# Kernel tuning notes

Measured on AMD Instinct MI355X. Metric: run time of the kernel, lower is better.

The kernel has to match this reference:

```python
import jax, jax.numpy as jnp
import numpy as np

H, K, D = 24, 2, 128          # query heads, kv heads, head_size
HIDDEN = H * D                # 3072
ROPE_THETA = 10000.0


def setup_inputs() -> dict:
    key = jax.random.key(0)
    ks = jax.random.split(key, 6)
    B, S = 2, 2048
    T = B * S
    hidden_states = jax.random.normal(ks[0], (T, HIDDEN), dtype=jnp.float32)
    w_qkv = jax.random.normal(ks[1], ((H + 2 * K) * D, HIDDEN), dtype=jnp.float32) * (HIDDEN ** -0.5)
    b_qkv = jax.random.normal(ks[2], ((H + 2 * K) * D,), dtype=jnp.float32) * 0.02
    w_o = jax.random.normal(ks[3], (HIDDEN, H * D), dtype=jnp.float32) * (HIDDEN ** -0.5)
    b_o = jax.random.normal(ks[4], (HIDDEN,), dtype=jnp.float32) * 0.02
    # rotary tables: positions restart per sequence (flash-varlen prefill layout)
    pos = jnp.tile(jnp.arange(S, dtype=jnp.float32), B)            # [T]
    inv_freq = 1.0 / (ROPE_THETA ** (jnp.arange(0, D, 2, dtype=jnp.float32) / D))  # [D/2]
    freqs = pos[:, None] * inv_freq[None, :]                        # [T, D/2]
    return {
        "hidden_states": hidden_states,
        "w_qkv": w_qkv, "b_qkv": b_qkv,
        "w_o": w_o, "b_o": b_o,
        "cos": jnp.cos(freqs), "sin": jnp.sin(freqs),
        "seq_len": S, "window": 1024,
    }


def _rope(x, cos, sin):
    # rotate-half (neox) style, as in TGI PositionRotaryEmbedding
    half = x.shape[-1] // 2
    x1, x2 = x[..., :half], x[..., half:]
    c, s = cos[:, None, :], sin[:, None, :]   # broadcast over head dim
    return jnp.concatenate([x1 * c - x2 * s, x2 * c + x1 * s], axis=-1)


def reference(hidden_states, w_qkv, b_qkv, w_o, b_o, cos, sin, seq_len, window):
    T = hidden_states.shape[0]
    B = T // seq_len
    scale = D ** -0.5

    # fused QKV projection
    qkv = hidden_states @ w_qkv.T + b_qkv                 # [T, (H+2K)*D]
    q = qkv[:, : H * D].reshape(T, H, D)
    kv = qkv[:, H * D:].reshape(T, 2, K, D)
    k, v = kv[:, 0], kv[:, 1]                             # [T, K, D]

    q = _rope(q, cos, sin)
    k = _rope(k, cos, sin)

    # GQA: expand kv heads to query heads
    groups = H // K
    qb = q.reshape(B, seq_len, H, D)
    kb = jnp.repeat(k.reshape(B, seq_len, K, D), groups, axis=2)  # [B,S,H,D]
    vb = jnp.repeat(v.reshape(B, seq_len, K, D), groups, axis=2)

    scores = jnp.einsum("bqhd,bkhd->bhqk", qb, kb) * scale        # [B,H,S,S]
    idx = jnp.arange(seq_len)
    delta = idx[:, None] - idx[None, :]
    mask = (delta >= 0) & (delta < window)                        # causal + sliding window
    scores = jnp.where(mask[None, None], scores, jnp.float32(-1e9))
    attn = jax.nn.softmax(scores, axis=-1)
    out = jnp.einsum("bhqk,bkhd->bqhd", attn, vb).reshape(T, H * D)
    return out @ w_o.T + b_o
```

## Files before the change

### kernel.cpp

```cpp
#include <hip/hip_runtime.h>
#include <hip/hip_bf16.h>

typedef __attribute__((ext_vector_type(8))) short bf16x8;
typedef __attribute__((ext_vector_type(4))) float f32x4;

__device__ __forceinline__ short f2bf_bits(float f) {
    __hip_bfloat16 h = __float2bfloat16(f);
    short s;
    __builtin_memcpy(&s, &h, 2);
    return s;
}

__device__ __forceinline__ float bf_bits2f(short s) {
    unsigned int u = ((unsigned int)(unsigned short)s) << 16;
    float f;
    __builtin_memcpy(&f, &u, 4);
    return f;
}

__device__ __forceinline__ bf16x8 load8(const float* p) {
    float4 a = *(const float4*)p;
    float4 b = *(const float4*)(p + 4);
    bf16x8 r;
    r[0] = f2bf_bits(a.x); r[1] = f2bf_bits(a.y);
    r[2] = f2bf_bits(a.z); r[3] = f2bf_bits(a.w);
    r[4] = f2bf_bits(b.x); r[5] = f2bf_bits(b.y);
    r[6] = f2bf_bits(b.z); r[7] = f2bf_bits(b.w);
    return r;
}
__device__ __forceinline__ bf16x8 load8(const __hip_bfloat16* p) {
    return *(const bf16x8*)p;
}

__device__ __forceinline__ void store_out(__hip_bfloat16* p, float v) {
    *p = __float2bfloat16(v);
}
__device__ __forceinline__ void store_out(float* p, float v) { *p = v; }

__global__ void cvt3_f32_bf16(const float* __restrict__ a, short* __restrict__ da, int na8,
                              const float* __restrict__ b, short* __restrict__ db, int nb8,
                              const float* __restrict__ c, short* __restrict__ dc, int nc8) {
    int i = blockIdx.x * 256 + threadIdx.x;
    if (i < na8) {
        *(bf16x8*)(da + (size_t)i * 8) = load8(a + (size_t)i * 8);
    } else if ((i -= na8) < nb8) {
        *(bf16x8*)(db + (size_t)i * 8) = load8(b + (size_t)i * 8);
    } else if ((i -= nb8) < nc8) {
        *(bf16x8*)(dc + (size_t)i * 8) = load8(c + (size_t)i * 8);
    }
}

#define GB_REG 65536

__device__ __forceinline__ int half_off(int buf, int half) {
    return buf * 32768 + half * 16384;
}

template <typename TC>
__global__ __launch_bounds__(512) void gemm256(
    const __hip_bfloat16* __restrict__ A, const __hip_bfloat16* __restrict__ B,
    const float* __restrict__ bias, TC* __restrict__ C, int M, int N, int K)
{
    __shared__ char smem[131072];

    const int tid  = threadIdx.x;
    const int lane = tid & 63;
    const int wid  = tid >> 6;
    const int quad = lane >> 4;
    const int m16  = lane & 15;
    const int wmg  = wid >> 2;
    const int wng  = wid & 3;
    const int bhalf = wng >> 1;
    const int bsub  = (wng & 1) * 4;

    const int gx  = gridDim.x;
    const int nwg = gx * gridDim.y;
    int lin = blockIdx.y * gx + blockIdx.x;
    if ((nwg & 7) == 0) {
        int q = nwg >> 3;
        lin = (lin & 7) * q + (lin >> 3);
    }
    const int bn = lin % gx, bm = lin / gx;
    const int mBase = bm * 256, nBase = bn * 256;

    const int roff = (m16 << 6) | ((quad * 16) ^ (((m16 >> 1) & 3) << 4));

    int r_s[2], c_s[2];
    #pragma unroll
    for (int l = 0; l < 2; ++l) {
        int sub = l * 8 + wid;
        int r16 = (tid >> 2) & 15;
        int cb  = ((tid & 3) * 16) ^ (((r16 >> 1) & 3) << 4);
        r_s[l] = (sub >> 1) * 16 + r16;
        c_s[l] = (sub & 1) * 32 + (cb >> 1);
    }

    const __hip_bfloat16* Ab = A + (size_t)mBase * K;
    const __hip_bfloat16* Bb = B + (size_t)nBase * K;

    auto stage = [&](int region, const __hip_bfloat16* base, int buf, int half, int tile) {
        const __hip_bfloat16* gb = base + (size_t)(half * 128) * K + tile * 64;
        #pragma unroll
        for (int l = 0; l < 2; ++l) {
            const __hip_bfloat16* g = gb + (size_t)r_s[l] * K + c_s[l];
            short* lb = (short*)(smem + region + half_off(buf, half) + l * 8192 + wid * 1024);
            __builtin_amdgcn_global_load_lds(
                (__attribute__((address_space(1))) void*)g,
                (__attribute__((address_space(3))) void*)lb, 16, 0, 0);
        }
    };

    f32x4 acc[8][4] = {};
    bf16x8 afr[4][2];
    bf16x8 bfr[2][2][2];

    auto LD_A = [&](int buf, int g) {
        const char* base = smem + half_off(buf, wmg) + (g ? 8192 : 0);
        #pragma unroll
        for (int m = 0; m < 4; ++m)
            #pragma unroll
            for (int ks = 0; ks < 2; ++ks)
                afr[m][ks] = *(const bf16x8*)(base + ((m * 2 + ks) << 10) + roff);
    };
    auto LD_B = [&](int buf, int g) {
        const char* base = smem + GB_REG + half_off(buf, bhalf) + ((bsub + g * 2) << 11);
        #pragma unroll
        for (int j = 0; j < 2; ++j)
            #pragma unroll
            for (int ks = 0; ks < 2; ++ks)
                bfr[g][j][ks] = *(const bf16x8*)(base + ((j * 2 + ks) << 10) + roff);
    };
    auto MM = [&](int mo, int g) {
        #pragma unroll
        for (int m = 0; m < 4; ++m)
            #pragma unroll
            for (int j = 0; j < 2; ++j)
                #pragma unroll
                for (int ks = 0; ks < 2; ++ks)
                    acc[mo + m][g * 2 + j] = __builtin_amdgcn_mfma_f32_16x16x32_bf16(
                        afr[m][ks], bfr[g][j][ks], acc[mo + m][g * 2 + j], 0, 0, 0);
    };

#define SBAR() __builtin_amdgcn_s_barrier()
#define WAIT_LGKM0() do { asm volatile("s_waitcnt lgkmcnt(0)" ::: "memory"); \
                          __builtin_amdgcn_sched_barrier(0); } while (0)
#define WAIT_VM4()   do { asm volatile("s_waitcnt vmcnt(4)"   ::: "memory"); \
                          __builtin_amdgcn_sched_barrier(0); } while (0)

    const int NT = K >> 6;

    stage(GB_REG, Bb, 0, 0, 0);
    stage(0,      Ab, 0, 0, 0);
    stage(GB_REG, Bb, 0, 1, 0);
    stage(0,      Ab, 0, 1, 0);
    stage(GB_REG, Bb, 1, 0, 1);
    stage(0,      Ab, 1, 0, 1);
    WAIT_VM4();
    SBAR();

    for (int i = 0; i < (NT >> 1); ++i) {
        const int to = 2 * i + 1;
        const int t2 = min(2 * i + 2, NT - 1);
        const int t3 = min(2 * i + 3, NT - 1);
        LD_A(0, 0); LD_B(0, 0);
        stage(GB_REG, Bb, 1, 1, to);
        SBAR(); WAIT_LGKM0();
        __builtin_amdgcn_s_setprio(1); MM(0, 0); __builtin_amdgcn_s_setprio(0);
        SBAR();
        LD_B(0, 1);
        stage(0, Ab, 1, 1, to);
        SBAR(); WAIT_LGKM0();
        __builtin_amdgcn_s_setprio(1); MM(0, 1); __builtin_amdgcn_s_setprio(0);
        SBAR();
        LD_A(0, 1);
        stage(GB_REG, Bb, 0, 0, t2);
        SBAR(); WAIT_LGKM0();
        __builtin_amdgcn_s_setprio(1); MM(4, 1); __builtin_amdgcn_s_setprio(0);
        SBAR();
        stage(0, Ab, 0, 0, t2);
        WAIT_VM4();
        SBAR();
        __builtin_amdgcn_s_setprio(1); MM(4, 0); __builtin_amdgcn_s_setprio(0);
        SBAR();
        LD_A(1, 0); LD_B(1, 0);
        stage(GB_REG, Bb, 0, 1, t2);
        SBAR(); WAIT_LGKM0();
        __builtin_amdgcn_s_setprio(1); MM(0, 0); __builtin_amdgcn_s_setprio(0);
        SBAR();
        LD_B(1, 1);
        stage(0, Ab, 0, 1, t2);
        SBAR(); WAIT_LGKM0();
        __builtin_amdgcn_s_setprio(1); MM(0, 1); __builtin_amdgcn_s_setprio(0);
        SBAR();
        LD_A(1, 1);
        stage(GB_REG, Bb, 1, 0, t3);
        SBAR(); WAIT_LGKM0();
        __builtin_amdgcn_s_setprio(1); MM(4, 1); __builtin_amdgcn_s_setprio(0);
        SBAR();
        stage(0, Ab, 1, 0, t3);
        WAIT_VM4();
        SBAR();
        __builtin_amdgcn_s_setprio(1); MM(4, 0); __builtin_amdgcn_s_setprio(0);
        SBAR();
    }

#undef SBAR
#undef WAIT_LGKM0
#undef WAIT_VM4

    float bv[4];
    #pragma unroll
    for (int j = 0; j < 4; ++j)
        bv[j] = bias[nBase + wng * 64 + j * 16 + m16];

    #pragma unroll
    for (int mf = 0; mf < 8; ++mf) {
        #pragma unroll
        for (int j = 0; j < 4; ++j) {
            const int col = nBase + wng * 64 + j * 16 + m16;
            #pragma unroll
            for (int r = 0; r < 4; ++r) {
                const int row = mBase + wmg * 128 + mf * 16 + quad * 4 + r;
                store_out(&C[(size_t)row * N + col], acc[mf][j][r] + bv[j]);
            }
        }
    }
}

#define LDSS 40

template <typename TA, typename TB, typename TC>
__global__ __launch_bounds__(256) void gemm_bt_bias(
    const TA* __restrict__ A, const TB* __restrict__ B,
    const float* __restrict__ bias, TC* __restrict__ C, int M, int N, int K)
{
    __shared__ short As[128 * LDSS];
    __shared__ short Bs[128 * LDSS];

    const int tid  = threadIdx.x;
    const int lane = tid & 63;
    const int wid  = tid >> 6;
    const int quad = lane >> 4;
    const int m16  = lane & 15;

    const int mBase = blockIdx.y * 128;
    const int nBase = blockIdx.x * 128;
    const int wm = (wid >> 1) * 64;
    const int wn = (wid & 1) * 64;

    f32x4 acc[4][4] = {};
    const int srow = tid >> 2;
    const int sgrp = (tid & 3) * 8;

    for (int kt = 0; kt < K; kt += 32) {
        __syncthreads();
        for (int p = 0; p < 2; ++p) {
            int r = srow + p * 64;
            *(bf16x8*)(&As[r * LDSS + sgrp]) =
                load8(A + (size_t)(mBase + r) * K + kt + sgrp);
            *(bf16x8*)(&Bs[r * LDSS + sgrp]) =
                load8(B + (size_t)(nBase + r) * K + kt + sgrp);
        }
        __syncthreads();

        bf16x8 afr[4], bfr[4];
        #pragma unroll
        for (int i = 0; i < 4; ++i)
            afr[i] = *(const bf16x8*)(&As[(wm + 16 * i + m16) * LDSS + quad * 8]);
        #pragma unroll
        for (int j = 0; j < 4; ++j)
            bfr[j] = *(const bf16x8*)(&Bs[(wn + 16 * j + m16) * LDSS + quad * 8]);
        #pragma unroll
        for (int i = 0; i < 4; ++i)
            #pragma unroll
            for (int j = 0; j < 4; ++j)
                acc[i][j] = __builtin_amdgcn_mfma_f32_16x16x32_bf16(
                    afr[i], bfr[j], acc[i][j], 0, 0, 0);
    }

    float bv[4];
    #pragma unroll
    for (int j = 0; j < 4; ++j)
        bv[j] = bias[nBase + wn + 16 * j + m16];

    #pragma unroll
    for (int i = 0; i < 4; ++i)
        #pragma unroll
        for (int j = 0; j < 4; ++j) {
            int col = nBase + wn + 16 * j + m16;
            #pragma unroll
            for (int r = 0; r < 4; ++r) {
                int row = mBase + wm + 16 * i + quad * 4 + r;
                store_out(&C[(size_t)row * N + col], acc[i][j][r] + bv[j]);
            }
        }
}

__global__ void rope_kernel(__hip_bfloat16* __restrict__ qkv,
                            const float* __restrict__ cosb,
                            const float* __restrict__ sinb, int T)
{
    int idx = blockIdx.x * 256 + threadIdx.x;
    int total = T * 26 * 8;
    if (idx >= total) return;
    int j = idx & 7;
    int h = (idx >> 3) % 26;
    int t = idx / (26 * 8);
    int col = (h < 24) ? h * 128 : 3072 + (h - 24) * 128;
    int d0 = j * 8;
    size_t base = (size_t)t * 3584 + col + d0;
    bf16x8 x1 = *(const bf16x8*)((const short*)qkv + base);
    bf16x8 x2 = *(const bf16x8*)((const short*)qkv + base + 64);
    float4 c0 = *(const float4*)(cosb + t * 64 + d0);
    float4 c1 = *(const float4*)(cosb + t * 64 + d0 + 4);
    float4 s0 = *(const float4*)(sinb + t * 64 + d0);
    float4 s1 = *(const float4*)(sinb + t * 64 + d0 + 4);
    float cc[8] = {c0.x, c0.y, c0.z, c0.w, c1.x, c1.y, c1.z, c1.w};
    float ss[8] = {s0.x, s0.y, s0.z, s0.w, s1.x, s1.y, s1.z, s1.w};
    bf16x8 o1, o2;
    #pragma unroll
    for (int i = 0; i < 8; ++i) {
        float f1 = bf_bits2f(x1[i]);
        float f2 = bf_bits2f(x2[i]);
        o1[i] = f2bf_bits(f1 * cc[i] - f2 * ss[i]);
        o2[i] = f2bf_bits(f2 * cc[i] + f1 * ss[i]);
    }
    *(bf16x8*)((short*)qkv + base)      = o1;
    *(bf16x8*)((short*)qkv + base + 64) = o2;
}

#define SM_SHIFT 12.0f
#define VPLANE 9248

__global__ __launch_bounds__(256, 3) void attn_kernel(
    const __hip_bfloat16* __restrict__ qkv,
    __hip_bfloat16* __restrict__ out,
    const int* __restrict__ seq_len_p, const int* __restrict__ window_p)
{
    const int S = seq_len_p[0];
    const int window = window_p[0];
    const float scale = 0.088388347648318447f;

    const int h   = blockIdx.y;
    const int kvh = h / 12;
    const int tid  = threadIdx.x;
    const int lane = tid & 63;
    const int wid  = tid >> 6;
    const int quad = lane >> 4;
    const int m16  = lane & 15;

    const int nbb = S >> 7;
    const int b   = blockIdx.x / nbb;
    const int ib  = blockIdx.x - b * nbb;
    const int qb  = (nbb - 1 - ib) << 7;
    const int qb_global = b * S + qb;

    __shared__ short Vt[2 * VPLANE];

    const size_t kvrow0 = (size_t)(b * S) * 3584 + 3072 + kvh * 128;

    bf16x8 qf[2][4];
    {
        const __hip_bfloat16* qp =
            qkv + (size_t)(qb_global + wid * 32 + m16) * 3584 + h * 128;
        #pragma unroll
        for (int qt = 0; qt < 2; ++qt)
            #pragma unroll
            for (int dc = 0; dc < 4; ++dc)
                qf[qt][dc] = *(const bf16x8*)(qp + qt * 16 * 3584 + dc * 32 + quad * 8);
    }

    f32x4 accO[2][8] = {};
    float lqt[2] = {0.f, 0.f};

    int ka0 = qb - window + 1;
    if (ka0 < 0) ka0 = 0;
    ka0 &= ~63;
    const int kend = qb + 128;
    const int niter = (kend - ka0) >> 6;

    const int jkey = tid & 31;
    const int gg0  = tid >> 5;
    const int phi_base = ((m16 >> 2) << 3) + (m16 & 3);

    for (int it = 0; it < niter; ++it) {
        const int kt = ka0 + it * 64;

        const __hip_bfloat16* vp =
            qkv + kvrow0 + (size_t)(kt + 2 * jkey) * 3584 + 256;
        bf16x8 va0 = *(const bf16x8*)(vp + gg0 * 8);
        bf16x8 vb0 = *(const bf16x8*)(vp + 3584 + gg0 * 8);
        bf16x8 va1 = *(const bf16x8*)(vp + (gg0 + 8) * 8);
        bf16x8 vb1 = *(const bf16x8*)(vp + 3584 + (gg0 + 8) * 8);
        __builtin_amdgcn_sched_barrier(0);

        __builtin_amdgcn_s_barrier();

        {
            short* pl = &Vt[(jkey >> 4) * VPLANE];
            const int colsh = 2 * (jkey & 15);
            #pragma unroll
            for (int i2 = 0; i2 < 8; ++i2) {
                unsigned dw0 = (unsigned)(unsigned short)va0[i2] |
                               ((unsigned)(unsigned short)vb0[i2] << 16);
                *(unsigned*)(pl + (gg0 * 8 + i2) * 72 + colsh + (gg0 & 1) * 32) = dw0;
            }
            #pragma unroll
            for (int i2 = 0; i2 < 8; ++i2) {
                unsigned dw1 = (unsigned)(unsigned short)va1[i2] |
                               ((unsigned)(unsigned short)vb1[i2] << 16);
                *(unsigned*)(pl + ((gg0 + 8) * 8 + i2) * 72 + colsh + ((gg0 + 8) & 1) * 32) = dw1;
            }
        }
        asm volatile("s_waitcnt lgkmcnt(0)" ::: "memory");
        __builtin_amdgcn_s_barrier();
        __builtin_amdgcn_sched_barrier(0);

        bf16x8 pf[2][2];

        #pragma unroll
        for (int kb = 0; kb < 2; ++kb) {
            const int ktb = kt + kb * 32;
            f32x4 sacc[2][2] = {};
            #pragma unroll
            for (int st = 0; st < 2; ++st) {
                const __hip_bfloat16* kp =
                    qkv + kvrow0 + (size_t)(ktb + phi_base + st * 4) * 3584 + quad * 8;
                #pragma unroll
                for (int dc = 0; dc < 4; ++dc) {
                    bf16x8 kf = *(const bf16x8*)(kp + dc * 32);
                    sacc[st][0] = __builtin_amdgcn_mfma_f32_16x16x32_bf16(
                        kf, qf[0][dc], sacc[st][0], 0, 0, 0);
                    sacc[st][1] = __builtin_amdgcn_mfma_f32_16x16x32_bf16(
                        kf, qf[1][dc], sacc[st][1], 0, 0, 0);
                }
            }

            #pragma unroll
            for (int qt = 0; qt < 2; ++qt) {
                const int qmin = qb + wid * 32 + qt * 16;
                bf16x8 pfv;
                float psum = 0.f;
                if (ktb <= qmin - 31 && ktb >= qmin + 16 - window) {
                    #pragma unroll
                    for (int st = 0; st < 2; ++st)
                        #pragma unroll
                        for (int r = 0; r < 4; ++r) {
                            float pp = __expf(fminf(
                                sacc[st][qt][r] * scale - SM_SHIFT, 80.f));
                            psum += pp;
                            pfv[st * 4 + r] = f2bf_bits(pp);
                        }
                } else {
                    const int dl_base = (qmin + m16) - (ktb + quad * 8);
                    #pragma unroll
                    for (int st = 0; st < 2; ++st)
                        #pragma unroll
                        for (int r = 0; r < 4; ++r) {
                            int dl = dl_base - st * 4 - r;
                            float pp = ((unsigned)dl < (unsigned)window)
                                ? __expf(fminf(sacc[st][qt][r] * scale - SM_SHIFT, 80.f))
                                : 0.f;
                            psum += pp;
                            pfv[st * 4 + r] = f2bf_bits(pp);
                        }
                }
                psum += __shfl_xor(psum, 16, 64);
                psum += __shfl_xor(psum, 32, 64);
                lqt[qt] += psum;
                pf[qt][kb] = pfv;
            }
        }

        __builtin_amdgcn_s_setprio(1);
        #pragma unroll
        for (int kb = 0; kb < 2; ++kb) {
            const short* pl = &Vt[kb * VPLANE];
            #pragma unroll
            for (int dt = 0; dt < 8; ++dt) {
                int row = dt * 16 + m16;
                bf16x8 vf = *(const bf16x8*)(pl + row * 72 + quad * 8 + ((row >> 3) & 1) * 32);
                accO[0][dt] = __builtin_amdgcn_mfma_f32_16x16x32_bf16(
                    pf[0][kb], vf, accO[0][dt], 0, 0, 0);
                accO[1][dt] = __builtin_amdgcn_mfma_f32_16x16x32_bf16(
                    pf[1][kb], vf, accO[1][dt], 0, 0, 0);
            }
        }
        __builtin_amdgcn_s_setprio(0);
    }

    #pragma unroll
    for (int qt = 0; qt < 2; ++qt) {
        float li[4];
        #pragma unroll
        for (int r = 0; r < 4; ++r)
            li[r] = 1.0f / __shfl(lqt[qt], quad * 4 + r, 64);
        #pragma unroll
        for (int r = 0; r < 4; ++r) {
            int t = qb_global + wid * 32 + qt * 16 + quad * 4 + r;
            __hip_bfloat16* op = out + (size_t)t * 3072 + h * 128 + m16;
            #pragma unroll
            for (int dt = 0; dt < 8; ++dt)
                op[dt * 16] = __float2bfloat16(accO[qt][dt][r] * li[r]);
        }
    }
}

extern "C" void kernel_launch(void* const* d_in, const int* in_sizes, int n_in,
                              void* d_out, int out_size, void* d_ws, size_t ws_size,
                              hipStream_t stream) {
    const float* hidden = (const float*)d_in[0];
    const float* w_qkv  = (const float*)d_in[1];
    const float* b_qkv  = (const float*)d_in[2];
    const float* w_o    = (const float*)d_in[3];
    const float* b_o    = (const float*)d_in[4];
    const float* cosb   = (const float*)d_in[5];
    const float* sinb   = (const float*)d_in[6];
    const int* seq_len_p = (const int*)d_in[7];
    const int* window_p  = (const int*)d_in[8];

    const int HID  = in_sizes[4];
    const int NQKV = in_sizes[2];
    const int T    = in_sizes[0] / HID;

    size_t off = 0;
    auto alloc = [&](size_t bytes) {
        char* p = (char*)d_ws + off;
        off = (off + bytes + 255) & ~(size_t)255;
        return p;
    };
    __hip_bfloat16* qkv      = (__hip_bfloat16*)alloc((size_t)T * NQKV * 2);
    __hip_bfloat16* attn_out = (__hip_bfloat16*)alloc((size_t)T * HID * 2);
    __hip_bfloat16* hid_bf = (__hip_bfloat16*)alloc((size_t)T * HID * 2);
    __hip_bfloat16* wq_bf  = (__hip_bfloat16*)alloc((size_t)NQKV * HID * 2);
    __hip_bfloat16* wo_bf  = (__hip_bfloat16*)alloc((size_t)HID * HID * 2);
    const bool pre = (ws_size >= off);
    const bool big = pre && (T % 256 == 0) && (NQKV % 256 == 0) &&
                     (HID % 256 == 0) && (HID % 64 == 0);

    dim3 blk(256);

    if (big) {
        int n8h = T * HID / 8, n8q = NQKV * HID / 8, n8o = HID * HID / 8;
        int n8 = n8h + n8q + n8o;
        cvt3_f32_bf16<<<dim3((n8 + 255) / 256), blk, 0, stream>>>(
            hidden, (short*)hid_bf, n8h, w_qkv, (short*)wq_bf, n8q,
            w_o, (short*)wo_bf, n8o);
        gemm256<__hip_bfloat16><<<dim3(NQKV / 256, T / 256), dim3(512), 0, stream>>>(
            hid_bf, wq_bf, b_qkv, qkv, T, NQKV, HID);
    } else {
        gemm_bt_bias<float, float, __hip_bfloat16>
            <<<dim3(NQKV / 128, T / 128), blk, 0, stream>>>(
            hidden, w_qkv, b_qkv, qkv, T, NQKV, HID);
    }

    int total = T * 26 * 8;
    rope_kernel<<<dim3((total + 255) / 256), blk, 0, stream>>>(qkv, cosb, sinb, T);

    attn_kernel<<<dim3(T / 128, 24), blk, 0, stream>>>(qkv, attn_out, seq_len_p, window_p);

    if (big) {
        gemm256<float><<<dim3(HID / 256, T / 256), dim3(512), 0, stream>>>(
            attn_out, wo_bf, b_o, (float*)d_out, T, HID, HID);
    } else {
        gemm_bt_bias<__hip_bfloat16, float, float>
            <<<dim3(HID / 128, T / 128), blk, 0, stream>>>(
            attn_out, w_o, b_o, (float*)d_out, T, HID, HID);
    }
}
```

Before: 470.5 us.

## Prefetch K fragments into registers and defer row-sum shuffles to end

The QK^T loop in the attention kernel now loads the K fragments for the first 32-key half before the barrier. It loads the second half's K fragments while the first half's softmax is computed, overlapping global-load latency with MFMA and exp work. The cross-lane shuffle reduction of the row sums moves out of the inner loop and runs once after all iterations. MFMA blocks are wrapped in setprio. More live registers (16 bf16x8 K fragments) could lower occupancy or cause spills.

After: 479.3 us. Within noise of the previous version (+1.9%).

```diff
diff --git a/kernel.cpp b/kernel.cpp
--- a/kernel.cpp
+++ b/kernel.cpp
@@ -392,6 +392,16 @@
         bf16x8 vb0 = *(const bf16x8*)(vp + 3584 + gg0 * 8);
         bf16x8 va1 = *(const bf16x8*)(vp + (gg0 + 8) * 8);
         bf16x8 vb1 = *(const bf16x8*)(vp + 3584 + (gg0 + 8) * 8);
+        bf16x8 kreg0[2][4];
+        {
+            const __hip_bfloat16* kp =
+                qkv + kvrow0 + (size_t)(kt + phi_base) * 3584 + quad * 8;
+            #pragma unroll
+            for (int st = 0; st < 2; ++st)
+                #pragma unroll
+                for (int dc = 0; dc < 4; ++dc)
+                    kreg0[st][dc] = *(const bf16x8*)(kp + (size_t)(st * 4) * 3584 + dc * 32);
+        }
         __builtin_amdgcn_sched_barrier(0);
 
         __builtin_amdgcn_s_barrier();
@@ -418,24 +428,79 @@
 
         bf16x8 pf[2][2];
 
-        #pragma unroll
-        for (int kb = 0; kb < 2; ++kb) {
-            const int ktb = kt + kb * 32;
-            f32x4 sacc[2][2] = {};
-            #pragma unroll
-            for (int st = 0; st < 2; ++st) {
-                const __hip_bfloat16* kp =
-                    qkv + kvrow0 + (size_t)(ktb + phi_base + st * 4) * 3584 + quad * 8;
+        f32x4 sacc0[2][2] = {};
+        __builtin_amdgcn_s_setprio(1);
+        #pragma unroll
+        for (int st = 0; st < 2; ++st)
+            #pragma unroll
+            for (int dc = 0; dc < 4; ++dc) {
+                sacc0[st][0] = __builtin_amdgcn_mfma_f32_16x16x32_bf16(
+                    kreg0[st][dc], qf[0][dc], sacc0[st][0], 0, 0, 0);
+                sacc0[st][1] = __builtin_amdgcn_mfma_f32_16x16x32_bf16(
+                    kreg0[st][dc], qf[1][dc], sacc0[st][1], 0, 0, 0);
+            }
+        __builtin_amdgcn_s_setprio(0);
+
+        bf16x8 kreg1[2][4];
+        {
+            const __hip_bfloat16* kp =
+                qkv + kvrow0 + (size_t)(kt + 32 + phi_base) * 3584 + quad * 8;
+            #pragma unroll
+            for (int st = 0; st < 2; ++st)
                 #pragma unroll
-                for (int dc = 0; dc < 4; ++dc) {
-                    bf16x8 kf = *(const bf16x8*)(kp + dc * 32);
-                    sacc[st][0] = __builtin_amdgcn_mfma_f32_16x16x32_bf16(
-                        kf, qf[0][dc], sacc[st][0], 0, 0, 0);
-                    sacc[st][1] = __builtin_amdgcn_mfma_f32_16x16x32_bf16(
-                        kf, qf[1][dc], sacc[st][1], 0, 0, 0);
-                }
-            }
-
+                for (int dc = 0; dc < 4; ++dc)
+                    kreg1[st][dc] = *(const bf16x8*)(kp + (size_t)(st * 4) * 3584 + dc * 32);
+        }
+        __builtin_amdgcn_sched_barrier(0);
+
+        #pragma unroll
+        for (int qt = 0; qt < 2; ++qt) {
+            const int qmin = qb + wid * 32 + qt * 16;
+            bf16x8 pfv;
+            float psum = 0.f;
+            if (kt <= qmin - 31 && kt >= qmin + 16 - window) {
+                #pragma unroll
+                for (int st = 0; st < 2; ++st)
+                    #pragma unroll
+                    for (int r = 0; r < 4; ++r) {
+                        float pp = __expf(fminf(
+                            sacc0[st][qt][r] * scale - SM_SHIFT, 80.f));
+                        psum += pp;
+                        pfv[st * 4 + r] = f2bf_bits(pp);
+                    }
+            } else {
+                const int dl_base = (qmin + m16) - (kt + quad * 8);
+                #pragma unroll
+                for (int st = 0; st < 2; ++st)
+                    #pragma unroll
+                    for (int r = 0; r < 4; ++r) {
+                        int dl = dl_base - st * 4 - r;
+                        float pp = ((unsigned)dl < (unsigned)window)
+                            ? __expf(fminf(sacc0[st][qt][r] * scale - SM_SHIFT, 80.f))
+                            : 0.f;
+                        psum += pp;
+                        pfv[st * 4 + r] = f2bf_bits(pp);
+                    }
+            }
+            lqt[qt] += psum;
+            pf[qt][0] = pfv;
+        }
+
+        f32x4 sacc1[2][2] = {};
+        __builtin_amdgcn_s_setprio(1);
+        #pragma unroll
+        for (int st = 0; st < 2; ++st)
+            #pragma unroll
+            for (int dc = 0; dc < 4; ++dc) {
+                sacc1[st][0] = __builtin_amdgcn_mfma_f32_16x16x32_bf16(
+                    kreg1[st][dc], qf[0][dc], sacc1[st][0], 0, 0, 0);
+                sacc1[st][1] = __builtin_amdgcn_mfma_f32_16x16x32_bf16(
+                    kreg1[st][dc], qf[1][dc], sacc1[st][1], 0, 0, 0);
+            }
+        __builtin_amdgcn_s_setprio(0);
+
+        {
+            const int ktb = kt + 32;
             #pragma unroll
             for (int qt = 0; qt < 2; ++qt) {
                 const int qmin = qb + wid * 32 + qt * 16;
@@ -447,7 +512,7 @@
                         #pragma unroll
                         for (int r = 0; r < 4; ++r) {
                             float pp = __expf(fminf(
-                                sacc[st][qt][r] * scale - SM_SHIFT, 80.f));
+                                sacc1[st][qt][r] * scale - SM_SHIFT, 80.f));
                             psum += pp;
                             pfv[st * 4 + r] = f2bf_bits(pp);
                         }
@@ -459,16 +524,14 @@
                         for (int r = 0; r < 4; ++r) {
                             int dl = dl_base - st * 4 - r;
                             float pp = ((unsigned)dl < (unsigned)window)
-                                ? __expf(fminf(sacc[st][qt][r] * scale - SM_SHIFT, 80.f))
+                                ? __expf(fminf(sacc1[st][qt][r] * scale - SM_SHIFT, 80.f))
                                 : 0.f;
                             psum += pp;
                             pfv[st * 4 + r] = f2bf_bits(pp);
                         }
                 }
-                psum += __shfl_xor(psum, 16, 64);
-                psum += __shfl_xor(psum, 32, 64);
                 lqt[qt] += psum;
-                pf[qt][kb] = pfv;
+                pf[qt][1] = pfv;
             }
         }
 
@@ -487,6 +550,12 @@
             }
         }
         __builtin_amdgcn_s_setprio(0);
+    }
+
+    #pragma unroll
+    for (int qt = 0; qt < 2; ++qt) {
+        lqt[qt] += __shfl_xor(lqt[qt], 16, 64);
+        lqt[qt] += __shfl_xor(lqt[qt], 32, 64);
     }
 
     #pragma unroll
```

## Double-buffer V tile in LDS and defer row-sum reduction to loop end

Applied to the files above, without the earlier changes.

Adds a second LDS buffer for the transposed V tile. The next tile's global V loads are issued before the QK/softmax compute and written into the alternate buffer after the PV MFMAs, which leaves one barrier per iteration instead of two. Separately, the per-iteration cross-lane shuffle reduction of the softmax sum is moved to after the loop, since the partial sums can be accumulated per lane first. This doubles LDS use and keeps the V prefetch in registers, which may lower occupancy.

Result: slower. 537.6 us (+14.3%).

```diff
diff --git a/kernel.cpp b/kernel.cpp
--- a/kernel.cpp
+++ b/kernel.cpp
@@ -355,7 +355,7 @@
     const int qb  = (nbb - 1 - ib) << 7;
     const int qb_global = b * S + qb;
 
-    __shared__ short Vt[2 * VPLANE];
+    __shared__ short Vt[4 * VPLANE];
 
     const size_t kvrow0 = (size_t)(b * S) * 3584 + 3072 + kvh * 128;
 
@@ -383,37 +383,48 @@
     const int gg0  = tid >> 5;
     const int phi_base = ((m16 >> 2) << 3) + (m16 & 3);
 
-    for (int it = 0; it < niter; ++it) {
-        const int kt = ka0 + it * 64;
-
+    const int wr_pl   = (jkey >> 4) * VPLANE;
+    const int wr_col  = 2 * (jkey & 15);
+
+    {
         const __hip_bfloat16* vp =
-            qkv + kvrow0 + (size_t)(kt + 2 * jkey) * 3584 + 256;
+            qkv + kvrow0 + (size_t)(ka0 + 2 * jkey) * 3584 + 256;
         bf16x8 va0 = *(const bf16x8*)(vp + gg0 * 8);
         bf16x8 vb0 = *(const bf16x8*)(vp + 3584 + gg0 * 8);
         bf16x8 va1 = *(const bf16x8*)(vp + (gg0 + 8) * 8);
         bf16x8 vb1 = *(const bf16x8*)(vp + 3584 + (gg0 + 8) * 8);
-        __builtin_amdgcn_sched_barrier(0);
-
-        __builtin_amdgcn_s_barrier();
-
-        {
-            short* pl = &Vt[(jkey >> 4) * VPLANE];
-            const int colsh = 2 * (jkey & 15);
-            #pragma unroll
-            for (int i2 = 0; i2 < 8; ++i2) {
-                unsigned dw0 = (unsigned)(unsigned short)va0[i2] |
-                               ((unsigned)(unsigned short)vb0[i2] << 16);
-                *(unsigned*)(pl + (gg0 * 8 + i2) * 72 + colsh + (gg0 & 1) * 32) = dw0;
-            }
-            #pragma unroll
-            for (int i2 = 0; i2 < 8; ++i2) {
-                unsigned dw1 = (unsigned)(unsigned short)va1[i2] |
-                               ((unsigned)(unsigned short)vb1[i2] << 16);
-                *(unsigned*)(pl + ((gg0 + 8) * 8 + i2) * 72 + colsh + ((gg0 + 8) & 1) * 32) = dw1;
-            }
+        short* pl = &Vt[wr_pl];
+        #pragma unroll
+        for (int i2 = 0; i2 < 8; ++i2) {
+            unsigned dw = (unsigned)(unsigned short)va0[i2] |
+                          ((unsigned)(unsigned short)vb0[i2] << 16);
+            *(unsigned*)(pl + (gg0 * 8 + i2) * 72 + wr_col + (gg0 & 1) * 32) = dw;
+        }
+        #pragma unroll
+        for (int i2 = 0; i2 < 8; ++i2) {
+            unsigned dw = (unsigned)(unsigned short)va1[i2] |
+                          ((unsigned)(unsigned short)vb1[i2] << 16);
+            *(unsigned*)(pl + ((gg0 + 8) * 8 + i2) * 72 + wr_col + ((gg0 + 8) & 1) * 32) = dw;
         }
         asm volatile("s_waitcnt lgkmcnt(0)" ::: "memory");
         __builtin_amdgcn_s_barrier();
+        __builtin_amdgcn_sched_barrier(0);
+    }
+
+    for (int it = 0; it < niter; ++it) {
+        const int kt  = ka0 + it * 64;
+        const int buf = it & 1;
+        const bool more = (it + 1 < niter);
+
+        bf16x8 va0, vb0, va1, vb1;
+        if (more) {
+            const __hip_bfloat16* vp =
+                qkv + kvrow0 + (size_t)(kt + 64 + 2 * jkey) * 3584 + 256;
+            va0 = *(const bf16x8*)(vp + gg0 * 8);
+            vb0 = *(const bf16x8*)(vp + 3584 + gg0 * 8);
+            va1 = *(const bf16x8*)(vp + (gg0 + 8) * 8);
+            vb1 = *(const bf16x8*)(vp + 3584 + (gg0 + 8) * 8);
+        }
         __builtin_amdgcn_sched_barrier(0);
 
         bf16x8 pf[2][2];
@@ -465,8 +476,6 @@
                             pfv[st * 4 + r] = f2bf_bits(pp);
                         }
                 }
-                psum += __shfl_xor(psum, 16, 64);
-                psum += __shfl_xor(psum, 32, 64);
                 lqt[qt] += psum;
                 pf[qt][kb] = pfv;
             }
@@ -475,7 +484,7 @@
         __builtin_amdgcn_s_setprio(1);
         #pragma unroll
         for (int kb = 0; kb < 2; ++kb) {
-            const short* pl = &Vt[kb * VPLANE];
+            const short* pl = &Vt[buf * 2 * VPLANE + kb * VPLANE];
             #pragma unroll
             for (int dt = 0; dt < 8; ++dt) {
                 int row = dt * 16 + m16;
@@ -487,6 +496,31 @@
             }
         }
         __builtin_amdgcn_s_setprio(0);
+
+        if (more) {
+            short* pl = &Vt[(buf ^ 1) * 2 * VPLANE + wr_pl];
+            #pragma unroll
+            for (int i2 = 0; i2 < 8; ++i2) {
+                unsigned dw = (unsigned)(unsigned short)va0[i2] |
+                              ((unsigned)(unsigned short)vb0[i2] << 16);
+                *(unsigned*)(pl + (gg0 * 8 + i2) * 72 + wr_col + (gg0 & 1) * 32) = dw;
+            }
+            #pragma unroll
+            for (int i2 = 0; i2 < 8; ++i2) {
+                unsigned dw = (unsigned)(unsigned short)va1[i2] |
+                              ((unsigned)(unsigned short)vb1[i2] << 16);
+                *(unsigned*)(pl + ((gg0 + 8) * 8 + i2) * 72 + wr_col + ((gg0 + 8) & 1) * 32) = dw;
+            }
+            asm volatile("s_waitcnt lgkmcnt(0)" ::: "memory");
+            __builtin_amdgcn_s_barrier();
+            __builtin_amdgcn_sched_barrier(0);
+        }
+    }
+
+    #pragma unroll
+    for (int qt = 0; qt < 2; ++qt) {
+        lqt[qt] += __shfl_xor(lqt[qt], 16, 64);
+        lqt[qt] += __shfl_xor(lqt[qt], 32, 64);
     }
 
     #pragma unroll
```

## Split attention block across 8 waves with 16 query rows each

Applied to the files above, without the earlier changes.

The attention kernel now runs 512 threads (8 waves) per 128-query block. Each wave owns 16 query rows instead of 32, which halves the Q-fragment, accumulator and score registers per wave. The V staging into shared memory is spread over twice as many threads, and the row-sum shuffle reduction moves out of the loop to run once at the end. The aim is more waves in flight to hide latency. In exchange, each K fragment loaded from global memory now feeds half as many MFMAs, so K traffic per block doubles.

After: 640.8 us. 36.2% more time.

```diff
diff --git a/kernel.cpp b/kernel.cpp
--- a/kernel.cpp
+++ b/kernel.cpp
@@ -332,7 +332,7 @@
 #define SM_SHIFT 12.0f
 #define VPLANE 9248
 
-__global__ __launch_bounds__(256, 3) void attn_kernel(
+__global__ __launch_bounds__(512, 4) void attn_kernel(
     const __hip_bfloat16* __restrict__ qkv,
     __hip_bfloat16* __restrict__ out,
     const int* __restrict__ seq_len_p, const int* __restrict__ window_p)
@@ -359,19 +359,17 @@
 
     const size_t kvrow0 = (size_t)(b * S) * 3584 + 3072 + kvh * 128;
 
-    bf16x8 qf[2][4];
+    bf16x8 qf[4];
     {
         const __hip_bfloat16* qp =
-            qkv + (size_t)(qb_global + wid * 32 + m16) * 3584 + h * 128;
-        #pragma unroll
-        for (int qt = 0; qt < 2; ++qt)
-            #pragma unroll
-            for (int dc = 0; dc < 4; ++dc)
-                qf[qt][dc] = *(const bf16x8*)(qp + qt * 16 * 3584 + dc * 32 + quad * 8);
-    }
-
-    f32x4 accO[2][8] = {};
-    float lqt[2] = {0.f, 0.f};
+            qkv + (size_t)(qb_global + wid * 16 + m16) * 3584 + h * 128;
+        #pragma unroll
+        for (int dc = 0; dc < 4; ++dc)
+            qf[dc] = *(const bf16x8*)(qp + dc * 32 + quad * 8);
+    }
+
+    f32x4 accO[8] = {};
+    float lq = 0.f;
 
     int ka0 = qb - window + 1;
     if (ka0 < 0) ka0 = 0;
@@ -380,48 +378,42 @@
     const int niter = (kend - ka0) >> 6;
 
     const int jkey = tid & 31;
-    const int gg0  = tid >> 5;
+    const int gg   = tid >> 5;
     const int phi_base = ((m16 >> 2) << 3) + (m16 & 3);
+
+    const int wr_pl  = (jkey >> 4) * VPLANE;
+    const int wr_col = 2 * (jkey & 15);
 
     for (int it = 0; it < niter; ++it) {
         const int kt = ka0 + it * 64;
 
         const __hip_bfloat16* vp =
             qkv + kvrow0 + (size_t)(kt + 2 * jkey) * 3584 + 256;
-        bf16x8 va0 = *(const bf16x8*)(vp + gg0 * 8);
-        bf16x8 vb0 = *(const bf16x8*)(vp + 3584 + gg0 * 8);
-        bf16x8 va1 = *(const bf16x8*)(vp + (gg0 + 8) * 8);
-        bf16x8 vb1 = *(const bf16x8*)(vp + 3584 + (gg0 + 8) * 8);
+        bf16x8 va = *(const bf16x8*)(vp + gg * 8);
+        bf16x8 vb = *(const bf16x8*)(vp + 3584 + gg * 8);
         __builtin_amdgcn_sched_barrier(0);
 
         __builtin_amdgcn_s_barrier();
 
         {
-            short* pl = &Vt[(jkey >> 4) * VPLANE];
-            const int colsh = 2 * (jkey & 15);
+            short* pl = &Vt[wr_pl];
             #pragma unroll
             for (int i2 = 0; i2 < 8; ++i2) {
-                unsigned dw0 = (unsigned)(unsigned short)va0[i2] |
-                               ((unsigned)(unsigned short)vb0[i2] << 16);
-                *(unsigned*)(pl + (gg0 * 8 + i2) * 72 + colsh + (gg0 & 1) * 32) = dw0;
-            }
-            #pragma unroll
-            for (int i2 = 0; i2 < 8; ++i2) {
-                unsigned dw1 = (unsigned)(unsigned short)va1[i2] |
-                               ((unsigned)(unsigned short)vb1[i2] << 16);
-                *(unsigned*)(pl + ((gg0 + 8) * 8 + i2) * 72 + colsh + ((gg0 + 8) & 1) * 32) = dw1;
+                unsigned dw = (unsigned)(unsigned short)va[i2] |
+                              ((unsigned)(unsigned short)vb[i2] << 16);
+                *(unsigned*)(pl + (gg * 8 + i2) * 72 + wr_col + (gg & 1) * 32) = dw;
             }
         }
         asm volatile("s_waitcnt lgkmcnt(0)" ::: "memory");
         __builtin_amdgcn_s_barrier();
         __builtin_amdgcn_sched_barrier(0);
 
-        bf16x8 pf[2][2];
+        bf16x8 pf[2];
 
         #pragma unroll
         for (int kb = 0; kb < 2; ++kb) {
             const int ktb = kt + kb * 32;
-            f32x4 sacc[2][2] = {};
+            f32x4 sacc[2] = {};
             #pragma unroll
             for (int st = 0; st < 2; ++st) {
                 const __hip_bfloat16* kp =
@@ -429,16 +421,13 @@
                 #pragma unroll
                 for (int dc = 0; dc < 4; ++dc) {
                     bf16x8 kf = *(const bf16x8*)(kp + dc * 32);
-                    sacc[st][0] = __builtin_amdgcn_mfma_f32_16x16x32_bf16(
-                        kf, qf[0][dc], sacc[st][0], 0, 0, 0);
-                    sacc[st][1] = __builtin_amdgcn_mfma_f32_16x16x32_bf16(
-                        kf, qf[1][dc], sacc[st][1], 0, 0, 0);
+                    sacc[st] = __builtin_amdgcn_mfma_f32_16x16x32_bf16(
+                        kf, qf[dc], sacc[st], 0, 0, 0);
                 }
             }
 
-            #pragma unroll
-            for (int qt = 0; qt < 2; ++qt) {
-                const int qmin = qb + wid * 32 + qt * 16;
+            {
+                const int qmin = qb + wid * 16;
                 bf16x8 pfv;
                 float psum = 0.f;
                 if (ktb <= qmin - 31 && ktb >= qmin + 16 - window) {
@@ -447,7 +436,7 @@
                         #pragma unroll
                         for (int r = 0; r < 4; ++r) {
                             float pp = __expf(fminf(
-                                sacc[st][qt][r] * scale - SM_SHIFT, 80.f));
+                                sacc[st][r] * scale - SM_SHIFT, 80.f));
                             psum += pp;
                             pfv[st * 4 + r] = f2bf_bits(pp);
                         }
@@ -459,16 +448,14 @@
                         for (int r = 0; r < 4; ++r) {
                             int dl = dl_base - st * 4 - r;
                             float pp = ((unsigned)dl < (unsigned)window)
-                                ? __expf(fminf(sacc[st][qt][r] * scale - SM_SHIFT, 80.f))
+                                ? __expf(fminf(sacc[st][r] * scale - SM_SHIFT, 80.f))
                                 : 0.f;
                             psum += pp;
                             pfv[st * 4 + r] = f2bf_bits(pp);
                         }
                 }
-                psum += __shfl_xor(psum, 16, 64);
-                psum += __shfl_xor(psum, 32, 64);
-                lqt[qt] += psum;
-                pf[qt][kb] = pfv;
+                lq += psum;
+                pf[kb] = pfv;
             }
         }
 
@@ -480,28 +467,28 @@
             for (int dt = 0; dt < 8; ++dt) {
                 int row = dt * 16 + m16;
                 bf16x8 vf = *(const bf16x8*)(pl + row * 72 + quad * 8 + ((row >> 3) & 1) * 32);
-                accO[0][dt] = __builtin_amdgcn_mfma_f32_16x16x32_bf16(
-                    pf[0][kb], vf, accO[0][dt], 0, 0, 0);
-                accO[1][dt] = __builtin_amdgcn_mfma_f32_16x16x32_bf16(
-                    pf[1][kb], vf, accO[1][dt], 0, 0, 0);
+                accO[dt] = __builtin_amdgcn_mfma_f32_16x16x32_bf16(
+                    pf[kb], vf, accO[dt], 0, 0, 0);
             }
         }
         __builtin_amdgcn_s_setprio(0);
     }
 
-    #pragma unroll
-    for (int qt = 0; qt < 2; ++qt) {
+    lq += __shfl_xor(lq, 16, 64);
+    lq += __shfl_xor(lq, 32, 64);
+
+    {
         float li[4];
         #pragma unroll
         for (int r = 0; r < 4; ++r)
-            li[r] = 1.0f / __shfl(lqt[qt], quad * 4 + r, 64);
+            li[r] = 1.0f / __shfl(lq, quad * 4 + r, 64);
         #pragma unroll
         for (int r = 0; r < 4; ++r) {
-            int t = qb_global + wid * 32 + qt * 16 + quad * 4 + r;
+            int t = qb_global + wid * 16 + quad * 4 + r;
             __hip_bfloat16* op = out + (size_t)t * 3072 + h * 128 + m16;
             #pragma unroll
             for (int dt = 0; dt < 8; ++dt)
-                op[dt * 16] = __float2bfloat16(accO[qt][dt][r] * li[r]);
+                op[dt * 16] = __float2bfloat16(accO[dt][r] * li[r]);
         }
     }
 }
@@ -557,7 +544,7 @@
     int total = T * 26 * 8;
     rope_kernel<<<dim3((total + 255) / 256), blk, 0, stream>>>(qkv, cosb, sinb, T);
 
-    attn_kernel<<<dim3(T / 128, 24), blk, 0, stream>>>(qkv, attn_out, seq_len_p, window_p);
+    attn_kernel<<<dim3(T / 128, 24), dim3(512), 0, stream>>>(qkv, attn_out, seq_len_p, window_p);
 
     if (big) {
         gemm256<float><<<dim3(HID / 256, T / 256), dim3(512), 0, stream>>>(
```
